# Performance work log

Hardware: AMD Instinct MI355X
Metric: run time of the kernel (lower is better)

## Reference

```python
import jax, jax.numpy as jnp
import numpy as np

N_NODES = 50000
N_EDGES = 800000
N_GRAPHS = 512
H = 64
F_NODE = 32
F_EDGE = 8
N_CLASSES = 10
EPS = 1e-5


def _bn(x, w, b):
    # BatchNorm1d in training mode: batch stats, biased variance
    m = jnp.mean(x, axis=0)
    v = jnp.mean(jnp.square(x - m), axis=0)
    return (x - m) * jax.lax.rsqrt(v + EPS) * w + b


def setup_inputs() -> dict:
    key = jax.random.key(0)
    ks = jax.random.split(key, 12)
    s = 0.02
    inp = {
        "x": jax.random.normal(ks[0], (N_NODES, F_NODE), jnp.float32),
        "edge_attr": jax.random.normal(ks[1], (N_EDGES, F_EDGE), jnp.float32),
        "edge_index": jax.random.randint(ks[2], (2, N_EDGES), 0, N_NODES),
        "batch": jnp.sort(jax.random.randint(ks[3], (N_NODES,), 0, N_GRAPHS)),
        "bn_feat_w": jnp.ones((F_NODE,), jnp.float32),
        "bn_feat_b": jnp.full((F_NODE,), 1e-4, jnp.float32),
        "Wn0": jax.random.normal(ks[4], (F_NODE, H), jnp.float32) * s,
        "bn0": jnp.zeros((H,), jnp.float32),
        "We0": jax.random.normal(ks[5], (2 * H + F_EDGE, H), jnp.float32) * s,
        "be0": jnp.zeros((H,), jnp.float32),
        "bns_w": jnp.ones((3, H), jnp.float32),
        "bns_b": jnp.full((3, H), 1e-4, jnp.float32),
        "Wn": jax.random.normal(ks[6], (3, H, H), jnp.float32) * s,
        "Wnb": jnp.zeros((3, H), jnp.float32),
        "We": jax.random.normal(ks[7], (3, 3 * H, H), jnp.float32) * s,
        "Web": jnp.zeros((3, H), jnp.float32),
        "bn_fc_w": jnp.ones((H,), jnp.float32),
        "bn_fc_b": jnp.full((H,), 1e-4, jnp.float32),
        "Wfc": jax.random.normal(ks[8], (H, H), jnp.float32) * s,
        "bfc": jnp.zeros((H,), jnp.float32),
        "bn_hid_w": jnp.ones((H,), jnp.float32),
        "bn_hid_b": jnp.full((H,), 1e-4, jnp.float32),
        "Wcls": jax.random.normal(ks[9], (H, N_CLASSES), jnp.float32) * s,
        "bcls": jnp.zeros((N_CLASSES,), jnp.float32),
    }
    return inp


def reference(x, edge_attr, edge_index, batch, bn_feat_w, bn_feat_b, Wn0, bn0,
              We0, be0, bns_w, bns_b, Wn, Wnb, We, Web, bn_fc_w, bn_fc_b,
              Wfc, bfc, bn_hid_w, bn_hid_b, Wcls, bcls):
    src, dst = edge_index[0], edge_index[1]
    n = x.shape[0]
    # symmetric GCN edge normalization (edge_norm=True)
    deg = jax.ops.segment_sum(jnp.ones_like(src, jnp.float32), dst, num_segments=n)
    dinv = jax.lax.rsqrt(jnp.maximum(deg, 1.0))
    norm = (dinv[src] * dinv[dst])[:, None]  # [E,1]

    # feature conv (gfn=True: linear transforms only, no propagation)
    h = _bn(x, bn_feat_w, bn_feat_b) @ Wn0 + bn0  # [N,H]
    e = (h[src] @ We0[:H] + h[dst] @ We0[H:2 * H]
         + edge_attr @ We0[2 * H:] + be0)         # [E,H]
    h = jax.nn.relu(h)
    e = jax.nn.relu(e)

    # stacked edge-gated GCN convs: BN -> conv(gather/scatter) -> ReLU
    for i in range(3):
        ht = _bn(h, bns_w[i], bns_b[i]) @ Wn[i] + Wnb[i]          # [N,H]
        hs = ht[src]                                               # [E,H] gather
        ei = (hs @ We[i, :H] + ht[dst] @ We[i, H:2 * H]
              + e @ We[i, 2 * H:] + Web[i])                        # [E,H]
        msg = norm * hs * jax.nn.sigmoid(ei)                       # edge-gated message
        h = jax.nn.relu(jax.ops.segment_sum(msg, dst, num_segments=n))

    # global_add_pool over graphs
    g = jax.ops.segment_sum(h, batch, num_segments=N_GRAPHS)       # [G,H]
    g = jax.nn.relu(_bn(g, bn_fc_w, bn_fc_b) @ Wfc + bfc)
    g = _bn(g, bn_hid_w, bn_hid_b) @ Wcls + bcls
    return jax.nn.log_softmax(g, axis=-1)
```

## Files before the change

### kernel.cpp

```cpp
#include <hip/hip_runtime.h>
#include <hip/hip_bf16.h>

#define N_NODESC 50000
#define N_EDGESC 800000
#define N_GRAPHSC 512
#define HDIM 64
#define FNODE 32
#define FEDGE 8
#define NCLS 10
#define BN_EPS 1e-5f
#define SCAN_B 256
#define SCAN_G 196
#define NPW 8

typedef __bf16 bf16x8 __attribute__((ext_vector_type(8)));
typedef float f32x4 __attribute__((ext_vector_type(4)));
typedef int i32x4 __attribute__((ext_vector_type(4)));
typedef unsigned int uint32;

static __device__ __forceinline__ float bcast(float v, int k) {
  return __uint_as_float(__builtin_amdgcn_readlane(__float_as_uint(v), k));
}
static __device__ __forceinline__ int bcast_i(int v, int k) {
  return __builtin_amdgcn_readlane(v, k);
}
static __device__ __forceinline__ unsigned short f2bu(float f) {
  __hip_bfloat16 b = __float2bfloat16(f);
  return *reinterpret_cast<unsigned short*>(&b);
}
static __device__ __forceinline__ float bu2f(unsigned short u) {
  __hip_bfloat16 b;
  *reinterpret_cast<unsigned short*>(&b) = u;
  return __bfloat162float(b);
}

__global__ void k_deg(const int* __restrict__ dst, uint32* __restrict__ degi) {
  int e = blockIdx.x * blockDim.x + threadIdx.x;
  if (e < N_EDGESC) atomicAdd(&degi[dst[e]], 1u);
}

__global__ void k_scan1(const uint32* __restrict__ degi, uint32* __restrict__ ptr,
                        uint32* __restrict__ bsum, float* __restrict__ dinv) {
  __shared__ uint32 s[SCAN_B];
  int t = threadIdx.x;
  int i = blockIdx.x * SCAN_B + t;
  uint32 v = (i < N_NODESC) ? degi[i] : 0u;
  if (i < N_NODESC) dinv[i] = rsqrtf(fmaxf((float)v, 1.0f));
  s[t] = v; __syncthreads();
  for (int off = 1; off < SCAN_B; off <<= 1) {
    uint32 x = (t >= off) ? s[t - off] : 0u; __syncthreads();
    s[t] += x; __syncthreads();
  }
  if (i < N_NODESC) ptr[i] = s[t] - v;
  if (t == SCAN_B - 1) bsum[blockIdx.x] = s[t];
}

__global__ void k_scan2(uint32* __restrict__ bsum) {
  __shared__ uint32 s[256];
  int t = threadIdx.x;
  uint32 v = (t < SCAN_G) ? bsum[t] : 0u;
  s[t] = v; __syncthreads();
  for (int off = 1; off < 256; off <<= 1) {
    uint32 x = (t >= off) ? s[t - off] : 0u; __syncthreads();
    s[t] += x; __syncthreads();
  }
  if (t < SCAN_G) bsum[t] = s[t] - v;
}

__global__ void k_scan3(uint32* __restrict__ ptr, const uint32* __restrict__ bsum) {
  int i = blockIdx.x * SCAN_B + threadIdx.x;
  if (i < N_NODESC) ptr[i] += bsum[blockIdx.x];
  if (blockIdx.x == 0 && threadIdx.x == 0) ptr[N_NODESC] = N_EDGESC;
}

template <int C>
__global__ void k_colstats(const float* __restrict__ in, int nrows, float* __restrict__ stats) {
  const int RPB = 256 / C;
  int tid = threadIdx.x;
  int col = tid % C;
  int rowOff = tid / C;
  float s = 0.f, s2 = 0.f;
  for (int r = blockIdx.x * RPB + rowOff; r < nrows; r += gridDim.x * RPB) {
    float v = in[r * C + col];
    s += v; s2 += v * v;
  }
  __shared__ float ls[256], ls2[256];
  ls[tid] = s; ls2[tid] = s2;
  __syncthreads();
  for (int off = 128; off >= C; off >>= 1) {
    if (tid < off) { ls[tid] += ls[tid + off]; ls2[tid] += ls2[tid + off]; }
    __syncthreads();
  }
  if (tid < C) {
    atomicAdd(&stats[tid], ls[tid]);
    atomicAdd(&stats[C + tid], ls2[tid]);
  }
}

template <int CIN, int COUT>
__global__ void k_foldbn(const float* __restrict__ stats, float invN,
                         const float* __restrict__ bnw, const float* __restrict__ bnb,
                         const float* __restrict__ W, const float* __restrict__ bias,
                         float* __restrict__ Wf, float* __restrict__ bf) {
  __shared__ float a[CIN], sh[CIN];
  int tid = threadIdx.x;
  if (tid < CIN) {
    float m = stats[tid] * invN;
    float v = stats[CIN + tid] * invN - m * m;
    float inv = rsqrtf(v + BN_EPS);
    float aa = bnw[tid] * inv;
    a[tid] = aa;
    sh[tid] = bnb[tid] - m * aa;
  }
  __syncthreads();
  for (int i = tid; i < CIN * COUT; i += 256) {
    int r = i / COUT;
    Wf[i] = a[r] * W[i];
  }
  if (tid < COUT) {
    float acc = bias ? bias[tid] : 0.f;
    for (int r = 0; r < CIN; ++r) acc += sh[r] * W[r * COUT + tid];
    bf[tid] = acc;
  }
}

template <int K, bool RELU>
__global__ void k_nodemm(const float* __restrict__ in, int nrows,
                         const float* __restrict__ W, const float* __restrict__ bias,
                         float* __restrict__ out) {
  int tid = threadIdx.x;
  int lane = tid & 63;
  float w[K];
#pragma unroll
  for (int k = 0; k < K; ++k) w[k] = W[k * 64 + lane];
  float bv = bias ? bias[lane] : 0.f;
  int wave = (blockIdx.x * blockDim.x + tid) >> 6;
  int nwaves = (gridDim.x * blockDim.x) >> 6;
  for (int r = wave; r < nrows; r += nwaves) {
    float rv = (lane < K) ? in[(size_t)r * K + lane] : 0.f;
    float acc = bv;
#pragma unroll
    for (int k = 0; k < K; ++k) acc = fmaf(bcast(rv, k), w[k], acc);
    if (RELU) acc = fmaxf(acc, 0.f);
    out[(size_t)r * 64 + lane] = acc;
  }
}

__global__ void __launch_bounds__(256, 2) k_stage0(
    const float* __restrict__ x, int nrows,
    const float* __restrict__ Wf, const float* __restrict__ bfv,
    const float* __restrict__ WA, const float* __restrict__ bA,
    const float* __restrict__ WB,
    float* __restrict__ h, unsigned short* __restrict__ hAb,
    unsigned short* __restrict__ hBb, float* __restrict__ stats) {
  __shared__ float st_s[64], st_s2[64];
  int tid = threadIdx.x;
  int lane = tid & 63;
  if (tid < 64) { st_s[tid] = 0.f; st_s2[tid] = 0.f; }
  __syncthreads();
  float w0[FNODE], wA[64], wB[64];
#pragma unroll
  for (int k = 0; k < FNODE; ++k) w0[k] = Wf[k * 64 + lane];
#pragma unroll
  for (int k = 0; k < 64; ++k) wA[k] = WA[k * 64 + lane];
#pragma unroll
  for (int k = 0; k < 64; ++k) wB[k] = WB[k * 64 + lane];
  float b0 = bfv[lane];
  float b2 = bA[lane];
  int wave = (blockIdx.x * blockDim.x + tid) >> 6;
  int nwaves = (gridDim.x * blockDim.x) >> 6;
  float s = 0.f, s2 = 0.f;
  for (int r = wave; r < nrows; r += nwaves) {
    float xv = (lane < FNODE) ? x[(size_t)r * FNODE + lane] : 0.f;
    float t0 = b0;
#pragma unroll
    for (int k = 0; k < FNODE; ++k) t0 = fmaf(bcast(xv, k), w0[k], t0);
    float aA = b2, aB = 0.f;
#pragma unroll
    for (int k = 0; k < 64; ++k) {
      float tb = bcast(t0, k);
      aA = fmaf(tb, wA[k], aA);
      aB = fmaf(tb, wB[k], aB);
    }
    float hv = fmaxf(t0, 0.f);
    h[(size_t)r * 64 + lane] = hv;
    s += hv; s2 += hv * hv;
    hAb[(size_t)r * 64 + lane] = f2bu(aA);
    hBb[(size_t)r * 64 + lane] = f2bu(aB);
  }
  atomicAdd(&st_s[lane], s);
  atomicAdd(&st_s2[lane], s2);
  __syncthreads();
  if (tid < 64) atomicAdd(&stats[tid], st_s[tid]);
  else if (tid < 128) atomicAdd(&stats[tid], st_s2[tid - 64]);
}

__global__ void __launch_bounds__(256, 2) k_node3(
    const float* __restrict__ h, int nrows,
    const float* __restrict__ stats, float invN,
    const float* __restrict__ bnw, const float* __restrict__ bnb,
    const float* __restrict__ Wn_i, const float* __restrict__ Wnb_i,
    const float* __restrict__ WA, const float* __restrict__ Wab,
    const float* __restrict__ WB,
    uint32* __restrict__ htP, unsigned short* __restrict__ htBb) {
  __shared__ float a_s[64], sh_s[64];
  int tid = threadIdx.x;
  int lane = tid & 63;
  if (tid < 64) {
    float m = stats[tid] * invN;
    float v = stats[64 + tid] * invN - m * m;
    float inv = rsqrtf(v + BN_EPS);
    float aa = bnw[tid] * inv;
    a_s[tid] = aa;
    sh_s[tid] = bnb[tid] - m * aa;
  }
  __syncthreads();
  float w1[64], w2[64], w3[64];
  float b1 = Wnb_i[lane];
#pragma unroll
  for (int k = 0; k < 64; ++k) {
    float raw = Wn_i[k * 64 + lane];
    w1[k] = a_s[k] * raw;
    b1 = fmaf(sh_s[k], raw, b1);
  }
#pragma unroll
  for (int k = 0; k < 64; ++k) w2[k] = WA[k * 64 + lane];
#pragma unroll
  for (int k = 0; k < 64; ++k) w3[k] = WB[k * 64 + lane];
  float b2 = Wab[lane];
  int cperm = (lane & 15) * 4 + (lane >> 4);
  int wave = (blockIdx.x * blockDim.x + tid) >> 6;
  int nwaves = (gridDim.x * blockDim.x) >> 6;
  for (int r = wave; r < nrows; r += nwaves) {
    float hv = h[(size_t)r * 64 + lane];
    float t1 = b1;
#pragma unroll
    for (int k = 0; k < 64; ++k) t1 = fmaf(bcast(hv, k), w1[k], t1);
    float t2 = b2;
    float t3 = 0.f;
#pragma unroll
    for (int k = 0; k < 64; ++k) {
      float tb = bcast(t1, k);
      t2 = fmaf(tb, w2[k], t2);
      t3 = fmaf(tb, w3[k], t3);
    }
    htP[(size_t)r * 64 + cperm] = ((uint32)f2bu(t2) << 16) | (uint32)f2bu(t1);
    htBb[(size_t)r * 64 + lane] = f2bu(t3);
  }
}

__global__ void k_scatedge(
    const int* __restrict__ src, const int* __restrict__ dst,
    const float* __restrict__ ea, const float* __restrict__ dinv,
    const uint32* __restrict__ ptr, uint32* __restrict__ cursor,
    const unsigned short* __restrict__ hAb, const unsigned short* __restrict__ hBb,
    const float* __restrict__ Wc,
    int* __restrict__ edge4,
    __hip_bfloat16* __restrict__ ebf) {
  int tid = threadIdx.x;
  int lane = tid & 63;
  float w[FEDGE];
#pragma unroll
  for (int k = 0; k < FEDGE; ++k) w[k] = Wc[k * 64 + lane];
  int wave = (blockIdx.x * blockDim.x + tid) >> 6;
  int nwaves = (gridDim.x * blockDim.x) >> 6;
  const int nquads = N_EDGESC / 4;
  int per = (nquads + nwaves - 1) / nwaves;
  int p0 = wave * per;
  int p1 = min(p0 + per, nquads);
  for (int pr = p0; pr < p1; ++pr) {
    int e = 4 * pr;
    int sv = (lane < 4) ? src[e + lane] : 0;
    int dv = (lane < 4) ? dst[e + lane] : 0;
    int s_j[4], d_j[4];
#pragma unroll
    for (int j = 0; j < 4; ++j) { s_j[j] = bcast_i(sv, j); d_j[j] = bcast_i(dv, j); }
    uint32 idx_l = 0;
    if (lane < 4) {
      uint32 rk = atomicAdd(&cursor[dv], 1u);
      idx_l = ptr[dv] + rk;
      i32x4 q;
      q.x = sv; q.y = dv;
      q.z = __float_as_int(dinv[sv] * dinv[dv]);
      q.w = 0;
      __builtin_nontemporal_store(q, reinterpret_cast<i32x4*>(edge4) + idx_l);
    }
    int i_j[4];
#pragma unroll
    for (int j = 0; j < 4; ++j) i_j[j] = bcast_i((int)idx_l, j);
    float eav = (lane < 32) ? ea[(size_t)e * FEDGE + lane] : 0.f;
    unsigned short a0 = hAb[(size_t)s_j[0] * 64 + lane], b0 = hBb[(size_t)d_j[0] * 64 + lane];
    unsigned short a1 = hAb[(size_t)s_j[1] * 64 + lane], b1 = hBb[(size_t)d_j[1] * 64 + lane];
    unsigned short a2 = hAb[(size_t)s_j[2] * 64 + lane], b2 = hBb[(size_t)d_j[2] * 64 + lane];
    unsigned short a3 = hAb[(size_t)s_j[3] * 64 + lane], b3 = hBb[(size_t)d_j[3] * 64 + lane];
    float acc0 = bu2f(a0) + bu2f(b0);
    float acc1 = bu2f(a1) + bu2f(b1);
    float acc2 = bu2f(a2) + bu2f(b2);
    float acc3 = bu2f(a3) + bu2f(b3);
#pragma unroll
    for (int k = 0; k < FEDGE; ++k) {
      acc0 = fmaf(bcast(eav, 0 * 8 + k), w[k], acc0);
      acc1 = fmaf(bcast(eav, 1 * 8 + k), w[k], acc1);
      acc2 = fmaf(bcast(eav, 2 * 8 + k), w[k], acc2);
      acc3 = fmaf(bcast(eav, 3 * 8 + k), w[k], acc3);
    }
    unsigned short* ob = reinterpret_cast<unsigned short*>(ebf);
    __builtin_nontemporal_store(f2bu(fmaxf(acc0, 0.f)), ob + (size_t)i_j[0] * 64 + lane);
    __builtin_nontemporal_store(f2bu(fmaxf(acc1, 0.f)), ob + (size_t)i_j[1] * 64 + lane);
    __builtin_nontemporal_store(f2bu(fmaxf(acc2, 0.f)), ob + (size_t)i_j[2] * 64 + lane);
    __builtin_nontemporal_store(f2bu(fmaxf(acc3, 0.f)), ob + (size_t)i_j[3] * 64 + lane);
  }
}

__global__ void __launch_bounds__(256, 4) k_conv_mfma(
    const __hip_bfloat16* __restrict__ ebf,
    const float* __restrict__ We2,
    const uint32* __restrict__ htP, const unsigned short* __restrict__ htBb,
    const int* __restrict__ edge4,
    const uint32* __restrict__ ptr,
    float* __restrict__ hout, float* __restrict__ stats,
    const int* __restrict__ batch, float* __restrict__ gout) {
  __shared__ float lds_acc[4][NPW * 65];
  __shared__ float lds_htB[4][NPW * 65];
  __shared__ float st_s[64], st_s2[64];
  const int tid = threadIdx.x;
  const int lane = tid & 63;
  const int w = tid >> 6;
  const int m = lane & 15;
  const int kg = lane >> 4;

  int wave = blockIdx.x * 4 + w;
  int n0 = wave * NPW;
  bool validw = (n0 < N_NODESC);

  if (stats) {
    if (tid < 64) { st_s[tid] = 0.f; st_s2[tid] = 0.f; }
    __syncthreads();
  }

  bf16x8 b[4][2];
#pragma unroll
  for (int t = 0; t < 4; ++t)
#pragma unroll
    for (int s = 0; s < 2; ++s)
#pragma unroll
      for (int j = 0; j < 8; ++j) {
        int k = s * 32 + kg * 8 + j;
        int c = t * 16 + m;
        b[t][s][j] = (__bf16)We2[k * 64 + c];
      }

  float* acc_l = lds_acc[w];
  float* htB_l = lds_htB[w];
#pragma unroll
  for (int r = 0; r < NPW; ++r) {
    acc_l[r * 65 + lane] = 0.f;
    htB_l[r * 65 + lane] = validw ? bu2f(htBb[(size_t)(n0 + r) * 64 + lane]) : 0.f;
  }

  int e0 = validw ? (int)ptr[n0] : 0;
  int eend = validw ? (int)ptr[n0 + NPW] : 0;
  int tb0 = e0 & ~15;

  float run[4] = {0.f, 0.f, 0.f, 0.f};
  int dcur = -1, rcur = 0;

  for (int tb = tb0; tb < eend; tb += 16) {
    const bf16x8* arow = reinterpret_cast<const bf16x8*>(ebf + (size_t)(tb + m) * 64 + kg * 8);
    bf16x8 a0 = __builtin_nontemporal_load(arow);
    bf16x8 a1 = __builtin_nontemporal_load(arow + 4);
    int rb = tb + kg * 4;
    int se[4], de[4];
    float ne[4];
#pragma unroll
    for (int j = 0; j < 4; ++j) {
      i32x4 q = *reinterpret_cast<const i32x4*>(edge4 + (size_t)(rb + j) * 4);
      se[j] = q.x; de[j] = q.y; ne[j] = __int_as_float(q.z);
    }
    uint4 pv[4];
#pragma unroll
    for (int j = 0; j < 4; ++j)
      pv[j] = *reinterpret_cast<const uint4*>(htP + (size_t)se[j] * 64 + m * 4);

    f32x4 acc[4];
#pragma unroll
    for (int t = 0; t < 4; ++t) {
      f32x4 z = {0.f, 0.f, 0.f, 0.f};
      acc[t] = __builtin_amdgcn_mfma_f32_16x16x32_bf16(a0, b[t][0], z, 0, 0, 0);
      acc[t] = __builtin_amdgcn_mfma_f32_16x16x32_bf16(a1, b[t][1], acc[t], 0, 0, 0);
    }

#pragma unroll
    for (int j = 0; j < 4; ++j) {
      int eidx = rb + j;
      bool valid = (eidx >= e0) && (eidx < eend);
      if (valid) {
        if (de[j] != dcur) {
          if (dcur >= 0) {
#pragma unroll
            for (int t = 0; t < 4; ++t) {
              atomicAdd(&acc_l[rcur * 65 + t * 16 + m], run[t]);
              run[t] = 0.f;
            }
          }
          dcur = de[j];
          rcur = dcur - n0;
        }
        uint32 pd[4] = {pv[j].x, pv[j].y, pv[j].z, pv[j].w};
#pragma unroll
        for (int t = 0; t < 4; ++t) {
          int c = t * 16 + m;
          float gate = acc[t][j] + bu2f((unsigned short)(pd[t] >> 16)) + htB_l[rcur * 65 + c];
          float sig = 1.0f / (1.0f + __expf(-gate));
          run[t] = fmaf(ne[j] * bu2f((unsigned short)(pd[t] & 0xffffu)), sig, run[t]);
        }
      }
    }
  }
  if (dcur >= 0) {
#pragma unroll
    for (int t = 0; t < 4; ++t)
      atomicAdd(&acc_l[rcur * 65 + t * 16 + m], run[t]);
  }

  if (gout) {
    if (validw) {
      int bcur = batch[n0];
      float racc = 0.f;
#pragma unroll
      for (int r = 0; r < NPW; ++r) {
        float v = fmaxf(acc_l[r * 65 + lane], 0.f);
        int bb = batch[n0 + r];
        if (bb != bcur) {
          atomicAdd(&gout[(size_t)bcur * 64 + lane], racc);
          racc = 0.f;
          bcur = bb;
        }
        racc += v;
      }
      atomicAdd(&gout[(size_t)bcur * 64 + lane], racc);
    }
  } else {
    float s = 0.f, s2 = 0.f;
    if (validw) {
#pragma unroll
      for (int r = 0; r < NPW; ++r) {
        float v = fmaxf(acc_l[r * 65 + lane], 0.f);
        hout[(size_t)(n0 + r) * 64 + lane] = v;
        s += v; s2 += v * v;
      }
    }
    if (stats) {
      atomicAdd(&st_s[lane], s);
      atomicAdd(&st_s2[lane], s2);
      __syncthreads();
      if (tid < 64) atomicAdd(&stats[tid], st_s[tid]);
      else if (tid < 128) atomicAdd(&stats[tid], st_s2[tid - 64]);
    }
  }
}

__global__ void k_cls(const float* __restrict__ g2, const float* __restrict__ Wc,
                      const float* __restrict__ bc, float* __restrict__ out) {
  int r = blockIdx.x * blockDim.x + threadIdx.x;
  if (r >= N_GRAPHSC) return;
  float z[NCLS];
#pragma unroll
  for (int c = 0; c < NCLS; ++c) z[c] = bc[c];
  for (int k = 0; k < HDIM; ++k) {
    float v = g2[r * HDIM + k];
#pragma unroll
    for (int c = 0; c < NCLS; ++c) z[c] = fmaf(v, Wc[k * NCLS + c], z[c]);
  }
  float m = z[0];
#pragma unroll
  for (int c = 1; c < NCLS; ++c) m = fmaxf(m, z[c]);
  float ssum = 0.f;
#pragma unroll
  for (int c = 0; c < NCLS; ++c) ssum += __expf(z[c] - m);
  float l = __logf(ssum);
#pragma unroll
  for (int c = 0; c < NCLS; ++c) out[r * NCLS + c] = z[c] - m - l;
}

extern "C" void kernel_launch(void* const* d_in, const int* in_sizes, int n_in,
                              void* d_out, int out_size, void* d_ws, size_t ws_size,
                              hipStream_t stream) {
  const float* x         = (const float*)d_in[0];
  const float* edge_attr = (const float*)d_in[1];
  const int*   ei        = (const int*)d_in[2];
  const int*   batch     = (const int*)d_in[3];
  const float* bn_feat_w = (const float*)d_in[4];
  const float* bn_feat_b = (const float*)d_in[5];
  const float* Wn0       = (const float*)d_in[6];
  const float* bn0       = (const float*)d_in[7];
  const float* We0       = (const float*)d_in[8];
  const float* be0       = (const float*)d_in[9];
  const float* bns_w     = (const float*)d_in[10];
  const float* bns_b     = (const float*)d_in[11];
  const float* Wn        = (const float*)d_in[12];
  const float* Wnb       = (const float*)d_in[13];
  const float* We        = (const float*)d_in[14];
  const float* Web       = (const float*)d_in[15];
  const float* bn_fc_w   = (const float*)d_in[16];
  const float* bn_fc_b   = (const float*)d_in[17];
  const float* Wfc       = (const float*)d_in[18];
  const float* bfc       = (const float*)d_in[19];
  const float* bn_hid_w  = (const float*)d_in[20];
  const float* bn_hid_b  = (const float*)d_in[21];
  const float* Wcls      = (const float*)d_in[22];
  const float* bcls      = (const float*)d_in[23];
  float* out = (float*)d_out;
  const int* src = ei;
  const int* dst = ei + N_EDGESC;

  char* p = (char*)d_ws;
  auto carve = [&](size_t bytes) {
    char* q = p;
    p += (bytes + 255) & ~(size_t)255;
    return q;
  };
  __hip_bfloat16* ebf = (__hip_bfloat16*)carve((size_t)N_EDGESC * 64 * 2);
  float* h    = (float*)carve((size_t)N_NODESC * 64 * 4);
  uint32* htP = (uint32*)carve((size_t)N_NODESC * 64 * 4);
  unsigned short* htBb = (unsigned short*)carve((size_t)N_NODESC * 64 * 2);
  unsigned short* hAb  = (unsigned short*)carve((size_t)N_NODESC * 64 * 2);
  unsigned short* hBb  = (unsigned short*)carve((size_t)N_NODESC * 64 * 2);
  float* dinv = (float*)carve((size_t)N_NODESC * 4);
  float* g    = (float*)carve((size_t)N_GRAPHSC * 64 * 4);
  float* g2   = (float*)carve((size_t)N_GRAPHSC * 64 * 4);
  float* stats= (float*)carve(6 * 128 * 4);
  float* Wf   = (float*)carve(64 * 64 * 4);
  float* bf   = (float*)carve(64 * 4);
  uint32* degi   = (uint32*)carve((size_t)50176 * 4);
  uint32* ptr    = (uint32*)carve((size_t)50176 * 4);
  uint32* cursor = (uint32*)carve((size_t)50176 * 4);
  uint32* bsum   = (uint32*)carve(256 * 4);
  int* edge4 = (int*)carve((size_t)N_EDGESC * 4 * 4);

  float* st_x  = stats;
  float* st_h0 = stats + 128;
  float* st_h1 = stats + 256;
  float* st_h2 = stats + 384;
  float* st_g  = stats + 512;
  float* st_g2 = stats + 640;

  hipMemsetAsync(degi, 0, (size_t)3 * 50176 * 4, stream);
  hipMemsetAsync(stats, 0, 6 * 128 * 4, stream);
  hipMemsetAsync(g, 0, N_GRAPHSC * 64 * 4, stream);

  k_deg<<<(N_EDGESC + 255) / 256, 256, 0, stream>>>(dst, degi);
  k_scan1<<<SCAN_G, SCAN_B, 0, stream>>>(degi, ptr, bsum, dinv);
  k_scan2<<<1, 256, 0, stream>>>(bsum);
  k_scan3<<<SCAN_G, SCAN_B, 0, stream>>>(ptr, bsum);

  k_colstats<FNODE><<<256, 256, 0, stream>>>(x, N_NODESC, st_x);
  k_foldbn<FNODE, HDIM><<<1, 256, 0, stream>>>(st_x, 1.f / N_NODESC, bn_feat_w, bn_feat_b, Wn0, bn0, Wf, bf);
  k_stage0<<<512, 256, 0, stream>>>(x, N_NODESC, Wf, bf, We0, be0, We0 + 64 * 64, h, hAb, hBb, st_h0);

  k_scatedge<<<1024, 256, 0, stream>>>(src, dst, edge_attr, dinv, ptr, cursor,
                                       hAb, hBb, We0 + 128 * 64, edge4, ebf);

  const int convBlocks = (N_NODESC / NPW + 3) / 4;
  float* inSlot[3]  = {st_h0, st_h1, st_h2};
  float* outSlot[3] = {st_h1, st_h2, nullptr};
  for (int i = 0; i < 3; ++i) {
    const float* WeI = We + (size_t)i * 192 * 64;
    k_node3<<<512, 256, 0, stream>>>(h, N_NODESC, inSlot[i], 1.f / N_NODESC,
                                     bns_w + i * 64, bns_b + i * 64,
                                     Wn + (size_t)i * 64 * 64, Wnb + i * 64,
                                     WeI, Web + i * 64, WeI + 64 * 64, htP, htBb);
    k_conv_mfma<<<convBlocks, 256, 0, stream>>>(ebf, WeI + 128 * 64, htP, htBb, edge4,
                                                ptr, h, outSlot[i],
                                                batch, (i == 2) ? g : nullptr);
  }

  k_colstats<HDIM><<<32, 256, 0, stream>>>(g, N_GRAPHSC, st_g);
  k_foldbn<HDIM, HDIM><<<1, 256, 0, stream>>>(st_g, 1.f / N_GRAPHSC, bn_fc_w, bn_fc_b, Wfc, bfc, Wf, bf);
  k_nodemm<HDIM, true><<<128, 256, 0, stream>>>(g, N_GRAPHSC, Wf, bf, g2);
  k_colstats<HDIM><<<32, 256, 0, stream>>>(g2, N_GRAPHSC, st_g2);
  k_foldbn<HDIM, NCLS><<<1, 256, 0, stream>>>(st_g2, 1.f / N_GRAPHSC, bn_hid_w, bn_hid_b, Wcls, bcls, Wf, bf);
  k_cls<<<(N_GRAPHSC + 255) / 256, 256, 0, stream>>>(g2, Wf, bf, out);
}
```

Baseline: 682.0 us.

## Pack edge records into 8 bytes and fuse tail BN stats with fold

The per-edge CSR record shrinks from 16 bytes (src, dst, norm, pad) to a packed 64-bit word. It holds the source index in 17 bits, the destination's row offset within the wave's 8-node group in 3 bits, and the norm as float bits. The conv kernel reads this record three times per forward pass, so halving it cuts gather traffic, and the destination comparison now uses the local row directly. Separately, the graph-level column statistics and BN weight folding are merged into one single-block kernel for each of the two head BNs, removing two launches and two stats buffers. The 17-bit source field limits node count to about 131k, which holds for this problem size.

Result: slower. 720.4 us (+5.6%).

```diff
diff --git a/kernel.cpp b/kernel.cpp
--- a/kernel.cpp
+++ b/kernel.cpp
@@ -15,7 +15,8 @@
 
 typedef __bf16 bf16x8 __attribute__((ext_vector_type(8)));
 typedef float f32x4 __attribute__((ext_vector_type(4)));
-typedef int i32x4 __attribute__((ext_vector_type(4)));
+typedef unsigned long long uint64;
+typedef unsigned long long u64x2 __attribute__((ext_vector_type(2)));
 typedef unsigned int uint32;
 
 static __device__ __forceinline__ float bcast(float v, int k) {
@@ -121,6 +122,48 @@
     float acc = bias ? bias[tid] : 0.f;
     for (int r = 0; r < CIN; ++r) acc += sh[r] * W[r * COUT + tid];
     bf[tid] = acc;
+  }
+}
+
+template <int C, int COUT>
+__global__ void k_statsfold(const float* __restrict__ in, int nrows,
+                            const float* __restrict__ bnw, const float* __restrict__ bnb,
+                            const float* __restrict__ W, const float* __restrict__ bias,
+                            float* __restrict__ Wf, float* __restrict__ bfo) {
+  __shared__ float a[C], sh[C];
+  __shared__ float ls[256], ls2[256];
+  int tid = threadIdx.x;
+  const int RPB = 256 / C;
+  int col = tid % C;
+  int rowOff = tid / C;
+  float s = 0.f, s2 = 0.f;
+  for (int r = rowOff; r < nrows; r += RPB) {
+    float v = in[(size_t)r * C + col];
+    s += v; s2 += v * v;
+  }
+  ls[tid] = s; ls2[tid] = s2;
+  __syncthreads();
+  for (int off = 128; off >= C; off >>= 1) {
+    if (tid < off) { ls[tid] += ls[tid + off]; ls2[tid] += ls2[tid + off]; }
+    __syncthreads();
+  }
+  if (tid < C) {
+    float m = ls[tid] / (float)nrows;
+    float v = ls2[tid] / (float)nrows - m * m;
+    float inv = rsqrtf(v + BN_EPS);
+    float aa = bnw[tid] * inv;
+    a[tid] = aa;
+    sh[tid] = bnb[tid] - m * aa;
+  }
+  __syncthreads();
+  for (int i = tid; i < C * COUT; i += 256) {
+    int r = i / COUT;
+    Wf[i] = a[r] * W[i];
+  }
+  if (tid < COUT) {
+    float acc = bias ? bias[tid] : 0.f;
+    for (int r = 0; r < C; ++r) acc += sh[r] * W[r * COUT + tid];
+    bfo[tid] = acc;
   }
 }
 
@@ -255,7 +298,7 @@
     const uint32* __restrict__ ptr, uint32* __restrict__ cursor,
     const unsigned short* __restrict__ hAb, const unsigned short* __restrict__ hBb,
     const float* __restrict__ Wc,
-    int* __restrict__ edge4,
+    uint64* __restrict__ edge8,
     __hip_bfloat16* __restrict__ ebf) {
   int tid = threadIdx.x;
   int lane = tid & 63;
@@ -279,11 +322,10 @@
     if (lane < 4) {
       uint32 rk = atomicAdd(&cursor[dv], 1u);
       idx_l = ptr[dv] + rk;
-      i32x4 q;
-      q.x = sv; q.y = dv;
-      q.z = __float_as_int(dinv[sv] * dinv[dv]);
-      q.w = 0;
-      __builtin_nontemporal_store(q, reinterpret_cast<i32x4*>(edge4) + idx_l);
+      float nf = dinv[sv] * dinv[dv];
+      uint64 rec = ((uint64)__float_as_uint(nf) << 32) |
+                   ((uint64)(dv & (NPW - 1)) << 17) | (uint64)(uint32)sv;
+      __builtin_nontemporal_store(rec, edge8 + idx_l);
     }
     int i_j[4];
 #pragma unroll
@@ -316,7 +358,7 @@
     const __hip_bfloat16* __restrict__ ebf,
     const float* __restrict__ We2,
     const uint32* __restrict__ htP, const unsigned short* __restrict__ htBb,
-    const int* __restrict__ edge4,
+    const uint64* __restrict__ edge8,
     const uint32* __restrict__ ptr,
     float* __restrict__ hout, float* __restrict__ stats,
     const int* __restrict__ batch, float* __restrict__ gout) {
@@ -363,19 +405,23 @@
   int tb0 = e0 & ~15;
 
   float run[4] = {0.f, 0.f, 0.f, 0.f};
-  int dcur = -1, rcur = 0;
+  int rcur = -1;
 
   for (int tb = tb0; tb < eend; tb += 16) {
     const bf16x8* arow = reinterpret_cast<const bf16x8*>(ebf + (size_t)(tb + m) * 64 + kg * 8);
     bf16x8 a0 = __builtin_nontemporal_load(arow);
     bf16x8 a1 = __builtin_nontemporal_load(arow + 4);
     int rb = tb + kg * 4;
-    int se[4], de[4];
+    u64x2 qa = *reinterpret_cast<const u64x2*>(edge8 + rb);
+    u64x2 qb = *reinterpret_cast<const u64x2*>(edge8 + rb + 2);
+    uint64 q[4] = {qa.x, qa.y, qb.x, qb.y};
+    int se[4], rd[4];
     float ne[4];
 #pragma unroll
     for (int j = 0; j < 4; ++j) {
-      i32x4 q = *reinterpret_cast<const i32x4*>(edge4 + (size_t)(rb + j) * 4);
-      se[j] = q.x; de[j] = q.y; ne[j] = __int_as_float(q.z);
+      se[j] = (int)(q[j] & 0x1FFFFu);
+      rd[j] = (int)((q[j] >> 17) & (NPW - 1));
+      ne[j] = __uint_as_float((uint32)(q[j] >> 32));
     }
     uint4 pv[4];
 #pragma unroll
@@ -395,16 +441,15 @@
       int eidx = rb + j;
       bool valid = (eidx >= e0) && (eidx < eend);
       if (valid) {
-        if (de[j] != dcur) {
-          if (dcur >= 0) {
+        if (rd[j] != rcur) {
+          if (rcur >= 0) {
 #pragma unroll
             for (int t = 0; t < 4; ++t) {
               atomicAdd(&acc_l[rcur * 65 + t * 16 + m], run[t]);
               run[t] = 0.f;
             }
           }
-          dcur = de[j];
-          rcur = dcur - n0;
+          rcur = rd[j];
         }
         uint32 pd[4] = {pv[j].x, pv[j].y, pv[j].z, pv[j].w};
 #pragma unroll
@@ -417,7 +462,7 @@
       }
     }
   }
-  if (dcur >= 0) {
+  if (rcur >= 0) {
 #pragma unroll
     for (int t = 0; t < 4; ++t)
       atomicAdd(&acc_l[rcur * 65 + t * 16 + m], run[t]);
@@ -529,24 +574,22 @@
   float* dinv = (float*)carve((size_t)N_NODESC * 4);
   float* g    = (float*)carve((size_t)N_GRAPHSC * 64 * 4);
   float* g2   = (float*)carve((size_t)N_GRAPHSC * 64 * 4);
-  float* stats= (float*)carve(6 * 128 * 4);
+  float* stats= (float*)carve(4 * 128 * 4);
   float* Wf   = (float*)carve(64 * 64 * 4);
   float* bf   = (float*)carve(64 * 4);
   uint32* degi   = (uint32*)carve((size_t)50176 * 4);
   uint32* ptr    = (uint32*)carve((size_t)50176 * 4);
   uint32* cursor = (uint32*)carve((size_t)50176 * 4);
   uint32* bsum   = (uint32*)carve(256 * 4);
-  int* edge4 = (int*)carve((size_t)N_EDGESC * 4 * 4);
+  uint64* edge8 = (uint64*)carve((size_t)N_EDGESC * 8);
 
   float* st_x  = stats;
   float* st_h0 = stats + 128;
   float* st_h1 = stats + 256;
   float* st_h2 = stats + 384;
-  float* st_g  = stats + 512;
-  float* st_g2 = stats + 640;
 
   hipMemsetAsync(degi, 0, (size_t)3 * 50176 * 4, stream);
-  hipMemsetAsync(stats, 0, 6 * 128 * 4, stream);
+  hipMemsetAsync(stats, 0, 4 * 128 * 4, stream);
   hipMemsetAsync(g, 0, N_GRAPHSC * 64 * 4, stream);
 
   k_deg<<<(N_EDGESC + 255) / 256, 256, 0, stream>>>(dst, degi);
@@ -559,7 +602,7 @@
   k_stage0<<<512, 256, 0, stream>>>(x, N_NODESC, Wf, bf, We0, be0, We0 + 64 * 64, h, hAb, hBb, st_h0);
 
   k_scatedge<<<1024, 256, 0, stream>>>(src, dst, edge_attr, dinv, ptr, cursor,
-                                       hAb, hBb, We0 + 128 * 64, edge4, ebf);
+                                       hAb, hBb, We0 + 128 * 64, edge8, ebf);
 
   const int convBlocks = (N_NODESC / NPW + 3) / 4;
   float* inSlot[3]  = {st_h0, st_h1, st_h2};
@@ -570,15 +613,13 @@
                                      bns_w + i * 64, bns_b + i * 64,
                                      Wn + (size_t)i * 64 * 64, Wnb + i * 64,
                                      WeI, Web + i * 64, WeI + 64 * 64, htP, htBb);
-    k_conv_mfma<<<convBlocks, 256, 0, stream>>>(ebf, WeI + 128 * 64, htP, htBb, edge4,
+    k_conv_mfma<<<convBlocks, 256, 0, stream>>>(ebf, WeI + 128 * 64, htP, htBb, edge8,
                                                 ptr, h, outSlot[i],
                                                 batch, (i == 2) ? g : nullptr);
   }
 
-  k_colstats<HDIM><<<32, 256, 0, stream>>>(g, N_GRAPHSC, st_g);
-  k_foldbn<HDIM, HDIM><<<1, 256, 0, stream>>>(st_g, 1.f / N_GRAPHSC, bn_fc_w, bn_fc_b, Wfc, bfc, Wf, bf);
+  k_statsfold<HDIM, HDIM><<<1, 256, 0, stream>>>(g, N_GRAPHSC, bn_fc_w, bn_fc_b, Wfc, bfc, Wf, bf);
   k_nodemm<HDIM, true><<<128, 256, 0, stream>>>(g, N_GRAPHSC, Wf, bf, g2);
-  k_colstats<HDIM><<<32, 256, 0, stream>>>(g2, N_GRAPHSC, st_g2);
-  k_foldbn<HDIM, NCLS><<<1, 256, 0, stream>>>(st_g2, 1.f / N_GRAPHSC, bn_hid_w, bn_hid_b, Wcls, bcls, Wf, bf);
+  k_statsfold<HDIM, NCLS><<<1, 256, 0, stream>>>(g2, N_GRAPHSC, bn_hid_w, bn_hid_b, Wcls, bcls, Wf, bf);
   k_cls<<<(N_GRAPHSC + 255) / 256, 256, 0, stream>>>(g2, Wf, bf, out);
 }
```
